# Kernel optimization log

Hardware: AMD Instinct MI355X
Metric: run time of the kernel (lower is better)

## Reference

```python
import jax, jax.numpy as jnp
import numpy as np

N, E, D, R, L, B, K = 10000, 160000, 256, 237, 6, 128, 33
EPS = 1e-6


def setup_inputs() -> dict:
    key = jax.random.key(0)
    ks = jax.random.split(key, 8)
    x = jax.random.uniform(ks[0], (N, D), dtype=jnp.float32)
    edge_index = jax.random.randint(ks[1], (2, E), 0, N)
    edge_type = jax.random.randint(ks[2], (E,), 0, R)
    batch = jax.random.randint(ks[3], (B, K, 3), 0, R)
    rel_embs = jax.random.normal(ks[4], (L, R, D), dtype=jnp.float32) * 0.02
    Ws = jax.random.normal(ks[5], (L, 13 * D, D), dtype=jnp.float32) * 0.02
    bs = jnp.zeros((L, D), dtype=jnp.float32)
    ln_scale = jnp.ones((L, D), dtype=jnp.float32)
    ln_bias = jnp.zeros((L, D), dtype=jnp.float32)
    relation_emb = jax.random.normal(ks[6], (R, D), dtype=jnp.float32) * 0.02
    return dict(x=x, rel_embs=rel_embs, Ws=Ws, bs=bs, ln_scale=ln_scale,
                ln_bias=ln_bias, relation_emb=relation_emb,
                edge_index=edge_index, edge_type=edge_type, batch=batch)


def _layer_norm(h, g, b, eps=1e-5):
    mu = jnp.mean(h, axis=-1, keepdims=True)
    var = jnp.var(h, axis=-1, keepdims=True)
    return (h - mu) * jax.lax.rsqrt(var + eps) * g + b


def _rgcn_conv(x, edge_index, edge_type, rel, W, b, g, be):
    # DistMult message + self-loop boundary, PNA aggregation, linear+LN+ReLU.
    n, d = x.shape
    src, dst = edge_index[0], edge_index[1]
    msg = x[src] * rel[edge_type]                       # [E, D]
    msg = jnp.concatenate([msg, x], axis=0)             # self-loop messages
    seg = jnp.concatenate([dst, jnp.arange(n)], axis=0)
    deg = jax.ops.segment_sum(jnp.ones((msg.shape[0],), jnp.float32), seg, n)  # >= 1
    inv_deg = 1.0 / deg[:, None]
    mean = jax.ops.segment_sum(msg, seg, n) * inv_deg
    sq_mean = jax.ops.segment_sum(msg * msg, seg, n) * inv_deg
    mx = jax.ops.segment_max(msg, seg, n)
    mn = jax.ops.segment_min(msg, seg, n)
    std = jnp.sqrt(jnp.clip(sq_mean - mean * mean, EPS))
    feats = jnp.concatenate([mean, mx, mn, std], axis=-1)          # [N, 4D]
    scale = jnp.log(deg)
    scale = scale / jnp.mean(scale)
    scales = jnp.stack([jnp.ones_like(scale), scale,
                        1.0 / jnp.clip(scale, 1e-2)], axis=-1)      # [N, 3]
    agg = (feats[:, :, None] * scales[:, None, :]).reshape(n, 12 * d)
    h = jnp.concatenate([agg, x], axis=-1) @ W + b                  # [N, D]
    return jax.nn.relu(_layer_norm(h, g, be))


def reference(x, rel_embs, Ws, bs, ln_scale, ln_bias, relation_emb,
              edge_index, edge_type, batch):
    for i in range(L):  # loop over layers (structurally distinct params)
        x = _rgcn_conv(x, edge_index, edge_type, rel_embs[i], Ws[i],
                       bs[i], ln_scale[i], ln_bias[i]) + x  # short_cut
    s = x[batch[:, :, 0]]                 # [B, K, D]
    r = relation_emb[batch[:, :, 1]]      # [B, K, D]
    t = x[batch[:, :, 2]]                 # [B, K, D]
    return jnp.sum(s * r * t, axis=-1)    # [B, K] DistMult scores
```

## Files before the change

### kernel.cpp

```cpp
#include <hip/hip_runtime.h>
#include <math.h>

typedef __attribute__((ext_vector_type(8))) _Float16 half8;
typedef __attribute__((ext_vector_type(4))) _Float16 half4;
typedef __attribute__((ext_vector_type(4))) float    floatx4;

#define N_NODES 10000
#define M_PAD   10112
#define MTILES  79
#define E_EDGES 160000
#define DIM     256
#define R_REL   237
#define L_LAYERS 6
#define B_BATCH 128
#define K_BATCH 33
#define K13     3328
#define WL_STRIDE 851968
#define EPS_STD 1e-6f
#define EPS_LN  1e-5f

__device__ __forceinline__ void gload16(const void* g, void* lds) {
    __builtin_amdgcn_global_load_lds(
        (const __attribute__((address_space(1))) unsigned int*)g,
        (__attribute__((address_space(3))) unsigned int*)lds, 16, 0, 0);
}

__global__ void hist_kernel(const int* __restrict__ dst, int* __restrict__ deg) {
    int e = blockIdx.x * blockDim.x + threadIdx.x;
    if (e < E_EDGES) atomicAdd(&deg[dst[e]], 1);
}

__global__ void scan_kernel(const int* __restrict__ deg_in, int* __restrict__ offs,
                            int* __restrict__ cursor, float* __restrict__ sum_log) {
    __shared__ int   part[1024];
    __shared__ float slog[1024];
    int t = threadIdx.x;
    const int CH = 10;
    int base = t * CH;
    int lsum = 0; float ls = 0.f;
    for (int j = 0; j < CH; j++) {
        int i = base + j;
        if (i < N_NODES) { int d = deg_in[i]; lsum += d; ls += logf((float)(d + 1)); }
    }
    part[t] = lsum; slog[t] = ls;
    __syncthreads();
    for (int off = 1; off < 1024; off <<= 1) {
        int v = (t >= off) ? part[t - off] : 0;
        __syncthreads();
        part[t] += v;
        __syncthreads();
    }
    int run = part[t] - lsum;
    for (int j = 0; j < CH; j++) {
        int i = base + j;
        if (i < N_NODES) { offs[i] = run; cursor[i] = run; run += deg_in[i]; }
    }
    __syncthreads();
    for (int off = 512; off > 0; off >>= 1) {
        if (t < off) slog[t] += slog[t + off];
        __syncthreads();
    }
    if (t == 0) sum_log[0] = slog[0];
}

__global__ void fill_kernel(const int* __restrict__ src, const int* __restrict__ dst,
                            const int* __restrict__ et, int* __restrict__ cursor,
                            int* __restrict__ csr_src, int* __restrict__ csr_et) {
    int e = blockIdx.x * blockDim.x + threadIdx.x;
    if (e < E_EDGES) {
        int d = dst[e];
        int p = atomicAdd(&cursor[d], 1);
        csr_src[p] = src[e];
        csr_et[p]  = et[e];
    }
}

__global__ void scales_kernel(const int* __restrict__ deg_in, const float* __restrict__ sum_log,
                              float* __restrict__ s1, float* __restrict__ s2) {
    int i = blockIdx.x * blockDim.x + threadIdx.x;
    if (i < N_NODES) {
        float mean = sum_log[0] * (1.0f / (float)N_NODES);
        float sc = logf((float)(deg_in[i] + 1)) / mean;
        s1[i] = sc;
        s2[i] = 1.0f / fmaxf(sc, 0.01f);
    }
}

__global__ void wt_kernel(const float* __restrict__ Ws, _Float16* __restrict__ Wt) {
    int idx = blockIdx.x * 256 + threadIdx.x;
    const int TOT = L_LAYERS * WL_STRIDE;
    if (idx >= TOT) return;
    int l = idx / WL_STRIDE;
    int r = idx - l * WL_STRIDE;
    int korig, n;
    if (r < 786432) {
        int sidx = r / 262144;
        int r2 = r - sidx * 262144;
        n = r2 >> 10;
        int k = r2 & 1023;
        korig = k * 3 + sidx;
    } else {
        int r2 = r - 786432;
        n = r2 >> 8;
        korig = 3072 + (r2 & 255);
    }
    Wt[idx] = (_Float16)Ws[(size_t)l * K13 * 256 + (size_t)korig * 256 + n];
}

__global__ void cvt_kernel(const float* __restrict__ in, _Float16* __restrict__ outp, int n) {
    int i = blockIdx.x * 256 + threadIdx.x;
    if (i < n) outp[i] = (_Float16)in[i];
}

__global__ void agg_kernel(const float* __restrict__ x, const _Float16* __restrict__ xh,
                           const _Float16* __restrict__ relh,
                           const int* __restrict__ offs, const int* __restrict__ deg_in,
                           const int* __restrict__ csr_src, const int* __restrict__ csr_et,
                           _Float16* __restrict__ feats) {
    int wid  = threadIdx.x >> 6;
    int lane = threadIdx.x & 63;
    int node = blockIdx.x * 4 + wid;
    if (node >= N_NODES) return;
    int half = lane >> 5;
    int sub  = lane & 31;
    int off = offs[node];
    int end = off + deg_in[node];
    const half8* xh8 = (const half8*)xh;
    const half8* rh8 = (const half8*)relh;

    float s_[8], q_[8], mx_[8], mn_[8];
    #pragma unroll
    for (int i = 0; i < 8; i++) { s_[i] = 0.f; q_[i] = 0.f; mx_[i] = -INFINITY; mn_[i] = INFINITY; }

    for (int base = off; base < end; base += 2) {
        int e = base + half;
        if (e < end) {
            int sN = csr_src[e];
            int et = csr_et[e];
            half8 xv = xh8[(size_t)sN * 32 + sub];
            half8 rv = rh8[(size_t)et * 32 + sub];
            #pragma unroll
            for (int i = 0; i < 8; i++) {
                float m = (float)xv[i] * (float)rv[i];
                s_[i] += m; q_[i] += m * m;
                mx_[i] = fmaxf(mx_[i], m);
                mn_[i] = fminf(mn_[i], m);
            }
        }
    }
    #pragma unroll
    for (int i = 0; i < 8; i++) {
        s_[i] += __shfl_xor(s_[i], 32);
        q_[i] += __shfl_xor(q_[i], 32);
        mx_[i] = fmaxf(mx_[i], __shfl_xor(mx_[i], 32));
        mn_[i] = fminf(mn_[i], __shfl_xor(mn_[i], 32));
    }
    const float4* xrow = (const float4*)(x + (size_t)node * 256);
    float4 xa = xrow[sub * 2], xb = xrow[sub * 2 + 1];
    float xs[8] = {xa.x, xa.y, xa.z, xa.w, xb.x, xb.y, xb.z, xb.w};
    #pragma unroll
    for (int i = 0; i < 8; i++) {
        s_[i] += xs[i]; q_[i] += xs[i] * xs[i];
        mx_[i] = fmaxf(mx_[i], xs[i]);
        mn_[i] = fminf(mn_[i], xs[i]);
    }
    float inv = 1.0f / (float)(end - off + 1);
    half8 hm, hx, hn, hs;
    #pragma unroll
    for (int i = 0; i < 8; i++) {
        float mean = s_[i] * inv;
        float sd = sqrtf(fmaxf(q_[i] * inv - mean * mean, EPS_STD));
        hm[i] = (_Float16)mean; hx[i] = (_Float16)mx_[i];
        hn[i] = (_Float16)mn_[i]; hs[i] = (_Float16)sd;
    }
    half8* fout = (half8*)(feats + (size_t)node * 1024);
    if (half == 0) {
        fout[0 * 32 + sub] = hm;
        fout[1 * 32 + sub] = hx;
    } else {
        fout[2 * 32 + sub] = hn;
        fout[3 * 32 + sub] = hs;
    }
}

__launch_bounds__(256, 3)
__global__ void gemm_kernel(const _Float16* __restrict__ feats, const _Float16* __restrict__ xh,
                            const _Float16* __restrict__ Wl, _Float16* __restrict__ hbuf) {
    __shared__ _Float16 sA[3][128 * 32];
    __shared__ _Float16 sB[3][128 * 32];

    int xcd = blockIdx.x & 7, loc = blockIdx.x >> 3;
    int lin = xcd * MTILES + loc;
    int sidx = lin & 3;
    int nh   = (lin >> 2) & 1;
    int m    = lin >> 3;
    const int i0 = m * 128;
    const int n0 = nh * 128;
    const int NS  = (sidx == 3) ? 8 : 32;
    const int nit = (NS - 2) / 3;

    const int tid   = threadIdx.x;
    const int lane  = tid & 63;
    const int w     = tid >> 6;
    const int wr    = w >> 1;
    const int wc    = w & 1;
    const int row_l = lane & 15;
    const int kq    = lane >> 4;

    int a_off[4], b_off[4];
    #pragma unroll
    for (int rf = 0; rf < 4; rf++) {
        int r = wr * 64 + rf * 16 + row_l;
        a_off[rf] = r * 32 + ((kq ^ ((r >> 1) & 3)) & 3) * 8;
    }
    #pragma unroll
    for (int cf = 0; cf < 4; cf++) {
        int n_ = wc * 64 + cf * 16 + row_l;
        b_off[cf] = n_ * 32 + ((kq ^ ((n_ >> 1) & 3)) & 3) * 8;
    }

    const char* a_src[2];
    const char* b_src[2];
    #pragma unroll
    for (int j = 0; j < 2; j++) {
        int rloc = j * 64 + w * 16 + (lane >> 2);
        int c = (lane & 3) ^ ((rloc >> 1) & 3);
        if (sidx < 3) {
            a_src[j] = (const char*)(feats + (size_t)(i0 + rloc) * 1024 + c * 8);
            b_src[j] = (const char*)(Wl + (size_t)sidx * 262144 + (size_t)(n0 + rloc) * 1024 + c * 8);
        } else {
            a_src[j] = (const char*)(xh + (size_t)(i0 + rloc) * 256 + c * 8);
            b_src[j] = (const char*)(Wl + 786432 + (size_t)(n0 + rloc) * 256 + c * 8);
        }
    }

    floatx4 acc[4][4];
    #pragma unroll
    for (int rf = 0; rf < 4; rf++)
        #pragma unroll
        for (int cf = 0; cf < 4; cf++)
            acc[rf][cf] = (floatx4){0.f, 0.f, 0.f, 0.f};

#define STAGE(BUF, S) do {                                                    \
    size_t koff_ = (size_t)(S) * 64;                      \
    gload16(a_src[0] + koff_, (char*)(&sA[BUF][0]) + (0 * 64 + w * 16) * 64); \
    gload16(a_src[1] + koff_, (char*)(&sA[BUF][0]) + (1 * 64 + w * 16) * 64); \
    gload16(b_src[0] + koff_, (char*)(&sB[BUF][0]) + (0 * 64 + w * 16) * 64); \
    gload16(b_src[1] + koff_, (char*)(&sB[BUF][0]) + (1 * 64 + w * 16) * 64); \
} while (0)

#define COMPUTE(CB) do {                                                      \
    half8 af[4], bf[4];                                                       \
    _Pragma("unroll")                                                         \
    for (int rf = 0; rf < 4; rf++) af[rf] = *(const half8*)(&sA[CB][a_off[rf]]); \
    _Pragma("unroll")                                                         \
    for (int cf = 0; cf < 4; cf++) bf[cf] = *(const half8*)(&sB[CB][b_off[cf]]); \
    _Pragma("unroll")                                                         \
    for (int rf = 0; rf < 4; rf++)                                            \
        _Pragma("unroll")                                                     \
        for (int cf = 0; cf < 4; cf++)                                        \
            acc[rf][cf] = __builtin_amdgcn_mfma_f32_16x16x32_f16(af[rf], bf[cf], acc[rf][cf], 0, 0, 0); \
} while (0)

#define STEP(S, CB, NB) do {                                                  \
    asm volatile("s_waitcnt vmcnt(4)" ::: "memory");                          \
    __builtin_amdgcn_s_barrier();                                             \
    STAGE(NB, (S) + 2);                                                       \
    COMPUTE(CB);                                                              \
} while (0)

    STAGE(0, 0);
    STAGE(1, 1);

    for (int it = 0; it < nit; ++it) {
        int s = it * 3;
        STEP(s + 0, 0, 2);
        STEP(s + 1, 1, 0);
        STEP(s + 2, 2, 1);
    }
    asm volatile("s_waitcnt vmcnt(4)" ::: "memory");
    __builtin_amdgcn_s_barrier();
    COMPUTE(0);
    asm volatile("s_waitcnt vmcnt(0)" ::: "memory");
    __builtin_amdgcn_s_barrier();
    COMPUTE(1);

#undef STAGE
#undef COMPUTE
#undef STEP

    _Float16* outb = hbuf + (size_t)sidx * M_PAD * 256;
    #pragma unroll
    for (int rf = 0; rf < 4; rf++) {
        #pragma unroll
        for (int j = 0; j < 4; j++) {
            int grow = i0 + wr * 64 + rf * 16 + kq * 4 + j;
            _Float16* orow = outb + (size_t)grow * 256 + n0 + wc * 64;
            #pragma unroll
            for (int cf = 0; cf < 4; cf++)
                orow[cf * 16 + row_l] = (_Float16)acc[rf][cf][j];
        }
    }
}

__global__ void ln_kernel(const _Float16* __restrict__ hbuf, const float* __restrict__ xin,
                          const float* __restrict__ s1a, const float* __restrict__ s2a,
                          const float* __restrict__ bvec, const float* __restrict__ gvec,
                          const float* __restrict__ evec, float* __restrict__ xout,
                          _Float16* __restrict__ xhout) {
    int wid = threadIdx.x >> 6, lane = threadIdx.x & 63;
    int row = blockIdx.x * 4 + wid;
    if (row >= N_NODES) return;
    const half4* p0 = (const half4*)(hbuf + (size_t)row * 256);
    const half4* p1 = (const half4*)(hbuf + (size_t)M_PAD * 256     + (size_t)row * 256);
    const half4* p2 = (const half4*)(hbuf + (size_t)M_PAD * 256 * 2 + (size_t)row * 256);
    const half4* p3 = (const half4*)(hbuf + (size_t)M_PAD * 256 * 3 + (size_t)row * 256);
    half4 h0 = p0[lane], h1 = p1[lane], h2 = p2[lane], h3 = p3[lane];
    float s1v = s1a[row], s2v = s2a[row];
    float4 bv = ((const float4*)bvec)[lane];
    float4 hv;
    hv.x = (float)h0.x + s1v * (float)h1.x + s2v * (float)h2.x + (float)h3.x + bv.x;
    hv.y = (float)h0.y + s1v * (float)h1.y + s2v * (float)h2.y + (float)h3.y + bv.y;
    hv.z = (float)h0.z + s1v * (float)h1.z + s2v * (float)h2.z + (float)h3.z + bv.z;
    hv.w = (float)h0.w + s1v * (float)h1.w + s2v * (float)h2.w + (float)h3.w + bv.w;
    float s = hv.x + hv.y + hv.z + hv.w;
    float qsq = hv.x*hv.x + hv.y*hv.y + hv.z*hv.z + hv.w*hv.w;
    #pragma unroll
    for (int off = 1; off < 64; off <<= 1) {
        s   += __shfl_xor(s, off);
        qsq += __shfl_xor(qsq, off);
    }
    float mu  = s * (1.0f / 256.0f);
    float var = qsq * (1.0f / 256.0f) - mu * mu;
    float rs  = rsqrtf(var + EPS_LN);
    float4 g = ((const float4*)gvec)[lane];
    float4 e = ((const float4*)evec)[lane];
    float4 xv = ((const float4*)(xin + (size_t)row * 256))[lane];
    float4 o;
    o.x = fmaxf((hv.x - mu) * rs * g.x + e.x, 0.f) + xv.x;
    o.y = fmaxf((hv.y - mu) * rs * g.y + e.y, 0.f) + xv.y;
    o.z = fmaxf((hv.z - mu) * rs * g.z + e.z, 0.f) + xv.z;
    o.w = fmaxf((hv.w - mu) * rs * g.w + e.w, 0.f) + xv.w;
    ((float4*)(xout + (size_t)row * 256))[lane] = o;
    half4 oh = { (_Float16)o.x, (_Float16)o.y, (_Float16)o.z, (_Float16)o.w };
    ((half4*)(xhout + (size_t)row * 256))[lane] = oh;
}

__global__ void score_kernel(const float* __restrict__ x, const float* __restrict__ remb,
                             const int* __restrict__ batch, float* __restrict__ out) {
    int wid = threadIdx.x >> 6, lane = threadIdx.x & 63;
    int g = blockIdx.x * 4 + wid;
    if (g >= B_BATCH * K_BATCH) return;
    int si = batch[g * 3 + 0], ri = batch[g * 3 + 1], ti = batch[g * 3 + 2];
    const float4* xs = (const float4*)(x + (size_t)si * 256);
    const float4* xr = (const float4*)(remb + (size_t)ri * 256);
    const float4* xt = (const float4*)(x + (size_t)ti * 256);
    float4 a = xs[lane], r = xr[lane], t = xt[lane];
    float p = a.x*r.x*t.x + a.y*r.y*t.y + a.z*r.z*t.z + a.w*r.w*t.w;
    #pragma unroll
    for (int off = 1; off < 64; off <<= 1) p += __shfl_xor(p, off);
    if (lane == 0) out[g] = p;
}

extern "C" void kernel_launch(void* const* d_in, const int* in_sizes, int n_in,
                              void* d_out, int out_size, void* d_ws, size_t ws_size,
                              hipStream_t stream) {
    const float* x_in     = (const float*)d_in[0];
    const float* rel_embs = (const float*)d_in[1];
    const float* Ws       = (const float*)d_in[2];
    const float* bs       = (const float*)d_in[3];
    const float* ln_s     = (const float*)d_in[4];
    const float* ln_b     = (const float*)d_in[5];
    const float* remb     = (const float*)d_in[6];
    const int*   eidx     = (const int*)d_in[7];
    const int*   etype    = (const int*)d_in[8];
    const int*   batch    = (const int*)d_in[9];
    float* out = (float*)d_out;

    char* wp = (char*)d_ws;
    size_t o = 0;
    auto alloc = [&](size_t bytes) { void* p = wp + o; o += (bytes + 255) & ~255ull; return p; };
    int*      deg_in  = (int*)     alloc((size_t)N_NODES * 4);
    int*      offs    = (int*)     alloc((size_t)N_NODES * 4);
    int*      cursor  = (int*)     alloc((size_t)N_NODES * 4);
    float*    s1      = (float*)   alloc((size_t)M_PAD * 4);
    float*    s2      = (float*)   alloc((size_t)M_PAD * 4);
    float*    sum_log = (float*)   alloc(256);
    int*      csr_src = (int*)     alloc((size_t)E_EDGES * 4);
    int*      csr_et  = (int*)     alloc((size_t)E_EDGES * 4);
    _Float16* feats   = (_Float16*)alloc((size_t)M_PAD * 1024 * 2);
    _Float16* Wt      = (_Float16*)alloc((size_t)L_LAYERS * WL_STRIDE * 2);
    _Float16* hbuf    = (_Float16*)alloc((size_t)4 * M_PAD * 256 * 2);
    float*    xb0     = (float*)   alloc((size_t)M_PAD * 256 * 4);
    float*    xb1     = (float*)   alloc((size_t)M_PAD * 256 * 4);
    _Float16* xh0     = (_Float16*)alloc((size_t)M_PAD * 256 * 2);
    _Float16* xh1     = (_Float16*)alloc((size_t)M_PAD * 256 * 2);
    _Float16* relh    = (_Float16*)alloc((size_t)L_LAYERS * R_REL * 256 * 2);

    const int* src  = eidx;
    const int* dstp = eidx + E_EDGES;

    hipMemsetAsync(deg_in, 0, (size_t)N_NODES * 4, stream);
    hist_kernel<<<(E_EDGES + 255) / 256, 256, 0, stream>>>(dstp, deg_in);
    scan_kernel<<<1, 1024, 0, stream>>>(deg_in, offs, cursor, sum_log);
    fill_kernel<<<(E_EDGES + 255) / 256, 256, 0, stream>>>(src, dstp, etype, cursor, csr_src, csr_et);
    scales_kernel<<<(N_NODES + 255) / 256, 256, 0, stream>>>(deg_in, sum_log, s1, s2);
    {
        const int TOT = L_LAYERS * WL_STRIDE;
        wt_kernel<<<(TOT + 255) / 256, 256, 0, stream>>>(Ws, Wt);
        const int RT = L_LAYERS * R_REL * 256;
        cvt_kernel<<<(RT + 255) / 256, 256, 0, stream>>>(rel_embs, relh, RT);
        const int XT = N_NODES * 256;
        cvt_kernel<<<(XT + 255) / 256, 256, 0, stream>>>(x_in, xh0, XT);
    }
    hipMemcpyAsync(xb0, x_in, (size_t)N_NODES * 256 * 4, hipMemcpyDeviceToDevice, stream);

    float* xc = xb0; float* xn = xb1;
    _Float16* xhc = xh0; _Float16* xhn = xh1;
    for (int l = 0; l < L_LAYERS; l++) {
        agg_kernel<<<(N_NODES + 3) / 4, 256, 0, stream>>>(
            xc, xhc, relh + (size_t)l * R_REL * 256,
            offs, deg_in, csr_src, csr_et, feats);
        gemm_kernel<<<632, 256, 0, stream>>>(
            feats, xhc, Wt + (size_t)l * WL_STRIDE, hbuf);
        ln_kernel<<<(N_NODES + 3) / 4, 256, 0, stream>>>(
            hbuf, xc, s1, s2, bs + (size_t)l * 256, ln_s + (size_t)l * 256,
            ln_b + (size_t)l * 256, xn, xhn);
        float* t = xc; xc = xn; xn = t;
        _Float16* th = xhc; xhc = xhn; xhn = th;
    }
    score_kernel<<<(B_BATCH * K_BATCH + 3) / 4, 256, 0, stream>>>(xc, remb, batch, out);
}
```

Before: 471.0 us.

## Deepen GEMM LDS pipeline to 4 stages with register double-buffered fragments

Restructures the fp16 MFMA GEMM main loop from a 3-buffer LDS ring to a 4-buffer ring, and prefetches the next k-slice's A/B fragments into a second register set while the current slice's MFMAs run. The aim is to hide global-to-LDS latency and LDS read latency behind matrix math. In exchange, LDS per block grows and register pressure rises, so launch bounds drop from 3 to 2 blocks per CU, lowering occupancy.

```diff
diff --git a/kernel.cpp b/kernel.cpp
--- a/kernel.cpp
+++ b/kernel.cpp
@@ -183,11 +183,11 @@
     }
 }
 
-__launch_bounds__(256, 3)
+__launch_bounds__(256, 2)
 __global__ void gemm_kernel(const _Float16* __restrict__ feats, const _Float16* __restrict__ xh,
                             const _Float16* __restrict__ Wl, _Float16* __restrict__ hbuf) {
-    __shared__ _Float16 sA[3][128 * 32];
-    __shared__ _Float16 sB[3][128 * 32];
+    __shared__ _Float16 sA[4][128 * 32];
+    __shared__ _Float16 sB[4][128 * 32];
 
     int xcd = blockIdx.x & 7, loc = blockIdx.x >> 3;
     int lin = xcd * MTILES + loc;
@@ -197,7 +197,7 @@
     const int i0 = m * 128;
     const int n0 = nh * 128;
     const int NS  = (sidx == 3) ? 8 : 32;
-    const int nit = (NS - 2) / 3;
+    const int nit4 = NS / 4 - 1;
 
     const int tid   = threadIdx.x;
     const int lane  = tid & 63;
@@ -241,6 +241,8 @@
         for (int cf = 0; cf < 4; cf++)
             acc[rf][cf] = (floatx4){0.f, 0.f, 0.f, 0.f};
 
+    half8 fa0[4], fb0[4], fa1[4], fb1[4];
+
 #define STAGE(BUF, S) do {                                                    \
     size_t koff_ = (size_t)(S) * 64;                      \
     gload16(a_src[0] + koff_, (char*)(&sA[BUF][0]) + (0 * 64 + w * 16) * 64); \
@@ -249,45 +251,62 @@
     gload16(b_src[1] + koff_, (char*)(&sB[BUF][0]) + (1 * 64 + w * 16) * 64); \
 } while (0)
 
-#define COMPUTE(CB) do {                                                      \
-    half8 af[4], bf[4];                                                       \
+#define FRAGR(CB, AF, BF) do {                                                \
     _Pragma("unroll")                                                         \
-    for (int rf = 0; rf < 4; rf++) af[rf] = *(const half8*)(&sA[CB][a_off[rf]]); \
+    for (int rf = 0; rf < 4; rf++) AF[rf] = *(const half8*)(&sA[CB][a_off[rf]]); \
     _Pragma("unroll")                                                         \
-    for (int cf = 0; cf < 4; cf++) bf[cf] = *(const half8*)(&sB[CB][b_off[cf]]); \
+    for (int cf = 0; cf < 4; cf++) BF[cf] = *(const half8*)(&sB[CB][b_off[cf]]); \
+} while (0)
+
+#define MFMA16(AF, BF) do {                                                   \
     _Pragma("unroll")                                                         \
     for (int rf = 0; rf < 4; rf++)                                            \
         _Pragma("unroll")                                                     \
         for (int cf = 0; cf < 4; cf++)                                        \
-            acc[rf][cf] = __builtin_amdgcn_mfma_f32_16x16x32_f16(af[rf], bf[cf], acc[rf][cf], 0, 0, 0); \
+            acc[rf][cf] = __builtin_amdgcn_mfma_f32_16x16x32_f16(AF[rf], BF[cf], acc[rf][cf], 0, 0, 0); \
 } while (0)
 
-#define STEP(S, CB, NB) do {                                                  \
-    asm volatile("s_waitcnt vmcnt(4)" ::: "memory");                          \
+#define STEP_STEADY(S, AF, BF, NAF, NBF) do {                                 \
+    MFMA16(AF, BF);                                                           \
+    STAGE(((S) + 3) & 3, (S) + 3);                                            \
+    asm volatile("s_waitcnt vmcnt(8)" ::: "memory");                          \
     __builtin_amdgcn_s_barrier();                                             \
-    STAGE(NB, (S) + 2);                                                       \
-    COMPUTE(CB);                                                              \
+    FRAGR(((S) + 1) & 3, NAF, NBF);                                           \
 } while (0)
 
     STAGE(0, 0);
     STAGE(1, 1);
-
-    for (int it = 0; it < nit; ++it) {
-        int s = it * 3;
-        STEP(s + 0, 0, 2);
-        STEP(s + 1, 1, 0);
-        STEP(s + 2, 2, 1);
-    }
+    STAGE(2, 2);
+    asm volatile("s_waitcnt vmcnt(8)" ::: "memory");
+    __builtin_amdgcn_s_barrier();
+    FRAGR(0, fa0, fb0);
+
+    for (int it = 0; it < nit4; ++it) {
+        int s = it * 4;
+        STEP_STEADY(s + 0, fa0, fb0, fa1, fb1);
+        STEP_STEADY(s + 1, fa1, fb1, fa0, fb0);
+        STEP_STEADY(s + 2, fa0, fb0, fa1, fb1);
+        STEP_STEADY(s + 3, fa1, fb1, fa0, fb0);
+    }
+    MFMA16(fa0, fb0);
+    STAGE(3, NS - 1);
+    asm volatile("s_waitcnt vmcnt(8)" ::: "memory");
+    __builtin_amdgcn_s_barrier();
+    FRAGR(1, fa1, fb1);
+    MFMA16(fa1, fb1);
     asm volatile("s_waitcnt vmcnt(4)" ::: "memory");
     __builtin_amdgcn_s_barrier();
-    COMPUTE(0);
+    FRAGR(2, fa0, fb0);
+    MFMA16(fa0, fb0);
     asm volatile("s_waitcnt vmcnt(0)" ::: "memory");
     __builtin_amdgcn_s_barrier();
-    COMPUTE(1);
+    FRAGR(3, fa1, fb1);
+    MFMA16(fa1, fb1);
 
 #undef STAGE
-#undef COMPUTE
-#undef STEP
+#undef FRAGR
+#undef MFMA16
+#undef STEP_STEADY
 
     _Float16* outb = hbuf + (size_t)sidx * M_PAD * 256;
     #pragma unroll
```

Measured after the change: 492.3 us. +4.5%, slower.
